# Kernel optimization log

Hardware: AMD Instinct MI355X
Metric: run time of the kernel (lower is better)

Reference implementation:

```python
import jax, jax.numpy as jnp
import numpy as np

D_MODEL = 2048
NUM_HEADS = 32
NUM_GROUPS = 8
D_K = D_MODEL // NUM_HEADS          # 64
HPG = NUM_HEADS // NUM_GROUPS       # heads per group = 4
B, S = 2, 2048


def setup_inputs() -> dict:
    key = jax.random.key(0)
    ks = jax.random.split(key, 9)
    w_scale = 0.02
    kv_dim = NUM_GROUPS * D_K
    return {
        "x":  jax.random.normal(ks[0], (B, S, D_MODEL), dtype=jnp.float32),
        "Wq": jax.random.normal(ks[1], (D_MODEL, D_MODEL), dtype=jnp.float32) * w_scale,
        "bq": jnp.zeros((D_MODEL,), dtype=jnp.float32),
        "Wk": jax.random.normal(ks[2], (D_MODEL, kv_dim), dtype=jnp.float32) * w_scale,
        "bk": jnp.zeros((kv_dim,), dtype=jnp.float32),
        "Wv": jax.random.normal(ks[3], (D_MODEL, kv_dim), dtype=jnp.float32) * w_scale,
        "bv": jnp.zeros((kv_dim,), dtype=jnp.float32),
        "Wo": jax.random.normal(ks[4], (D_MODEL, D_MODEL), dtype=jnp.float32) * w_scale,
        "bo": jnp.zeros((D_MODEL,), dtype=jnp.float32),
    }


def reference(x, Wq, bq, Wk, bk, Wv, bv, Wo, bo):
    b, s, _ = x.shape
    # projections (torch Linear math: x @ W^T + b, here weights stored as (in,out))
    Q = (x @ Wq + bq).reshape(b, s, NUM_HEADS, D_K).transpose(0, 2, 1, 3)   # [B,H,S,dk]
    Kg = (x @ Wk + bk).reshape(b, s, NUM_GROUPS, D_K).transpose(0, 2, 1, 3)  # [B,G,S,dk]
    Vg = (x @ Wv + bv).reshape(b, s, NUM_GROUPS, D_K).transpose(0, 2, 1, 3)
    # repeat_interleave K/V over head dim to full head count
    K = jnp.repeat(Kg, HPG, axis=1)  # [B,H,S,dk]
    V = jnp.repeat(Vg, HPG, axis=1)
    scores = jnp.einsum("bhqd,bhkd->bhqk", Q, K) / np.sqrt(D_K).astype(np.float32)
    attn = jax.nn.softmax(scores, axis=-1)
    out = jnp.einsum("bhqk,bhkd->bhqd", attn, V)               # [B,H,S,dk]
    out = out.transpose(0, 2, 1, 3).reshape(b, s, D_MODEL)
    out = out @ Wo + bo
    # module returns grouped K,V cache: K[:, ::HPG] == Kg
    return out, (Kg, Vg)
```

## Files before the change

kernel.cpp:

```cpp
#include <hip/hip_runtime.h>
#include <hip/hip_bf16.h>
#include <stdint.h>

#define S_LEN 2048
#define DM    2048
#define NH    32
#define NG    8
#define DK    64
#define BATCH 2
#define MROWS (BATCH*S_LEN)
#define NQKV  3072
#define SSCALE 0.18033688f

typedef __bf16 bf16x8 __attribute__((ext_vector_type(8)));
typedef short  s16x8  __attribute__((ext_vector_type(8)));
typedef float  f32x4  __attribute__((ext_vector_type(4)));
typedef unsigned int u32x4 __attribute__((ext_vector_type(4)));

__device__ __forceinline__ unsigned short f2b(float f) {
    unsigned int x = __float_as_uint(f);
    unsigned int r = (x + 0x7fffu + ((x >> 16) & 1u)) >> 16;
    return (unsigned short)r;
}
__device__ __forceinline__ bf16x8 ld8(const unsigned short* p) {
    return *(const bf16x8*)p;
}
__device__ __forceinline__ s16x8 cvt8(const float* p) {
    f32x4 a = *(const f32x4*)p;
    f32x4 b = *(const f32x4*)(p + 4);
    s16x8 o;
#pragma unroll
    for (int j = 0; j < 4; j++) { o[j] = (short)f2b(a[j]); o[4 + j] = (short)f2b(b[j]); }
    return o;
}
__device__ __forceinline__ void gl_lds(const unsigned short* g, unsigned short* l) {
    __builtin_amdgcn_global_load_lds(
        (const __attribute__((address_space(1))) unsigned int*)g,
        (__attribute__((address_space(3))) unsigned int*)l, 16, 0, 0);
}
__device__ __forceinline__ void wait_vm4() {
    asm volatile("s_waitcnt vmcnt(4)" ::: "memory");
}
__device__ __forceinline__ void wait_vm0() {
    asm volatile("s_waitcnt vmcnt(0)" ::: "memory");
}
__device__ __forceinline__ void bar() {
    __builtin_amdgcn_sched_barrier(0);
    __builtin_amdgcn_s_barrier();
    __builtin_amdgcn_sched_barrier(0);
}

#define TCVT 4096
#define TQ   4096
#define TK   1024
#define TV   1024
#define TO   4096
#define TB   12
#define NPREP (TCVT+TQ+TK+TV+TO+TB)
__global__ __launch_bounds__(256) void prep_fused(
    const float* __restrict__ x,
    const float* __restrict__ Wq, const float* __restrict__ Wk,
    const float* __restrict__ Wv, const float* __restrict__ Wo,
    const float* __restrict__ bq, const float* __restrict__ bk,
    const float* __restrict__ bv,
    unsigned short* __restrict__ xb,
    unsigned short* __restrict__ WqkvT, unsigned short* __restrict__ WoT,
    float* __restrict__ bqkv) {
    __shared__ float t[32][33];
    int bid = blockIdx.x;
    const int tx = threadIdx.x, ty = threadIdx.y;
    const int flat = ty * 32 + tx;
    if (bid < TCVT) {
        size_t id = (size_t)bid * 256 + flat;
        *(s16x8*)&xb[id * 8] = cvt8(x + id * 8);
        return;
    }
    bid -= TCVT;
    const float* in; unsigned short* out; int C, bx, by;
    if (bid < TQ) { in = Wq; out = WqkvT; C = DM; bx = bid & 63; by = bid >> 6; }
    else if ((bid -= TQ) < TK) { in = Wk; out = WqkvT + (size_t)2048 * DM; C = 512; bx = bid & 15; by = bid >> 4; }
    else if ((bid -= TK) < TV) { in = Wv; out = WqkvT + (size_t)2560 * DM; C = 512; bx = bid & 15; by = bid >> 4; }
    else if ((bid -= TV) < TO) { in = Wo; out = WoT; C = DM; bx = bid & 63; by = bid >> 6; }
    else {
        int i = (bid - TO) * 256 + flat;
        if (i < 2048) bqkv[i] = bq[i];
        else if (i < 2560) bqkv[i] = bk[i - 2048];
        else if (i < 3072) bqkv[i] = bv[i - 2560];
        return;
    }
    const int R = DM;
    int c0 = bx * 32, r0 = by * 32;
#pragma unroll
    for (int i = 0; i < 4; i++)
        t[ty + i * 8][tx] = in[(size_t)(r0 + ty + i * 8) * C + c0 + tx];
    __syncthreads();
#pragma unroll
    for (int i = 0; i < 4; i++)
        out[(size_t)(c0 + ty + i * 8) * R + r0 + tx] = f2b(t[tx][ty + i * 8]);
}

__device__ __forceinline__ void xcd_remap(int gx, int* bx, int* by) {
    int nwg = gx * (int)gridDim.y;
    int flat = (int)blockIdx.y * gx + (int)blockIdx.x;
    int wgid = (flat & 7) * (nwg >> 3) + (flat >> 3);
    *bx = wgid % gx;
    *by = wgid / gx;
}

__global__ __launch_bounds__(256, 3) void gemm_qkv(const unsigned short* __restrict__ A,
                                                const unsigned short* __restrict__ Bt,
                                                const float* __restrict__ bias,
                                                unsigned short* __restrict__ Qb,
                                                float* __restrict__ Kg, float* __restrict__ Vg,
                                                unsigned short* __restrict__ Kb,
                                                unsigned short* __restrict__ Vtb) {
    __shared__ alignas(16) unsigned short As[3][128 * 32];
    __shared__ alignas(16) unsigned short Bs[3][128 * 32];
    const int K = DM;
    const int tid = threadIdx.x;
    int bx, by;
    xcd_remap(NQKV / 128, &bx, &by);
    const int n0 = bx * 128, m0 = by * 128;
    const int w = tid >> 6, lane = tid & 63;
    const int ln15 = lane & 15, quad = lane >> 4;
    const int wm = (w >> 1) * 64, wn = (w & 1) * 64;
    const int xq = (quad ^ ((ln15 >> 1) & 3)) * 8;
    f32x4 acc[4][4] = {};

#define GSTAGE(k0v, buf) do {                                                    \
    _Pragma("unroll")                                                            \
    for (int i = 0; i < 2; ++i) {                                                \
        int s = w * 128 + i * 64 + lane;             \
        int r = s >> 2, cb = (s & 3) ^ ((r >> 1) & 3);                           \
        gl_lds(&A[(size_t)(m0 + r) * K + (k0v) + cb * 8],                        \
               &As[buf][(w * 128 + i * 64) * 8]);                                \
        gl_lds(&Bt[(size_t)(n0 + r) * K + (k0v) + cb * 8],                       \
               &Bs[buf][(w * 128 + i * 64) * 8]);                                \
    } } while (0)

    GSTAGE(0, 0);
    GSTAGE(32, 1);
    int cur = 0;
    for (int k0 = 0; k0 < K; k0 += 32) {
        if (k0 + 32 < K) wait_vm4(); else wait_vm0();
        bar();
        if (k0 + 64 < K) {
            int nb = cur + 2; if (nb >= 3) nb -= 3;
            GSTAGE(k0 + 64, nb);
        }
        bf16x8 af[4], bfr[4];
#pragma unroll
        for (int mt = 0; mt < 4; mt++)
            af[mt] = ld8(&As[cur][(wm + mt * 16 + ln15) * 32 + xq]);
#pragma unroll
        for (int nt = 0; nt < 4; nt++)
            bfr[nt] = ld8(&Bs[cur][(wn + nt * 16 + ln15) * 32 + xq]);
        __builtin_amdgcn_s_setprio(1);
#pragma unroll
        for (int mt = 0; mt < 4; mt++)
#pragma unroll
            for (int nt = 0; nt < 4; nt++)
                acc[mt][nt] = __builtin_amdgcn_mfma_f32_16x16x32_bf16(af[mt], bfr[nt], acc[mt][nt], 0, 0, 0);
        __builtin_amdgcn_s_setprio(0);
        cur = (cur + 1 == 3) ? 0 : cur + 1;
    }
#undef GSTAGE
#pragma unroll
    for (int nt = 0; nt < 4; nt++) {
        int col = n0 + wn + nt * 16 + ln15;
        float bv = bias[col];
#pragma unroll
        for (int mt = 0; mt < 4; mt++) {
            int row0 = m0 + wm + mt * 16 + quad * 4;
#pragma unroll
            for (int r = 0; r < 4; r++) {
                float val = acc[mt][nt][r] + bv;
                int row = row0 + r;
                int b = row >> 11, s = row & 2047;
                if (col < 2048) {
                    Qb[(size_t)row * DM + col] = f2b(val * SSCALE);
                } else if (col < 2560) {
                    int gc = col - 2048, g = gc >> 6, d = gc & 63;
                    size_t idx = (((size_t)(b * NG + g) * S_LEN + s) << 6) + d;
                    Kg[idx] = val;
                    Kb[idx] = f2b(val);
                } else {
                    int gc = col - 2560, g = gc >> 6, d = gc & 63;
                    Vg[(((size_t)(b * NG + g) * S_LEN + s) << 6) + d] = val;
                    Vtb[((size_t)(b * NG + g) * DK + d) * S_LEN + s] = f2b(val);
                }
            }
        }
    }
}

__global__ __launch_bounds__(256, 3) void gemm_o(const unsigned short* __restrict__ A,
                                              const unsigned short* __restrict__ Bt,
                                              const float* __restrict__ bias,
                                              float* __restrict__ C) {
    __shared__ alignas(16) unsigned short As[3][128 * 32];
    __shared__ alignas(16) unsigned short Bs[3][128 * 32];
    const int K = DM, N = DM;
    const int tid = threadIdx.x;
    int bx, by;
    xcd_remap(DM / 128, &bx, &by);
    const int n0 = bx * 128, m0 = by * 128;
    const int w = tid >> 6, lane = tid & 63;
    const int ln15 = lane & 15, quad = lane >> 4;
    const int wm = (w >> 1) * 64, wn = (w & 1) * 64;
    const int xq = (quad ^ ((ln15 >> 1) & 3)) * 8;
    f32x4 acc[4][4] = {};

#define GSTAGE(k0v, buf) do {                                                    \
    _Pragma("unroll")                                                            \
    for (int i = 0; i < 2; ++i) {                                                \
        int s = w * 128 + i * 64 + lane;                                         \
        int r = s >> 2, cb = (s & 3) ^ ((r >> 1) & 3);                           \
        gl_lds(&A[(size_t)(m0 + r) * K + (k0v) + cb * 8],                        \
               &As[buf][(w * 128 + i * 64) * 8]);                                \
        gl_lds(&Bt[(size_t)(n0 + r) * K + (k0v) + cb * 8],                       \
               &Bs[buf][(w * 128 + i * 64) * 8]);                                \
    } } while (0)

    GSTAGE(0, 0);
    GSTAGE(32, 1);
    int cur = 0;
    for (int k0 = 0; k0 < K; k0 += 32) {
        if (k0 + 32 < K) wait_vm4(); else wait_vm0();
        bar();
        if (k0 + 64 < K) {
            int nb = cur + 2; if (nb >= 3) nb -= 3;
            GSTAGE(k0 + 64, nb);
        }
        bf16x8 af[4], bfr[4];
#pragma unroll
        for (int mt = 0; mt < 4; mt++)
            af[mt] = ld8(&As[cur][(wm + mt * 16 + ln15) * 32 + xq]);
#pragma unroll
        for (int nt = 0; nt < 4; nt++)
            bfr[nt] = ld8(&Bs[cur][(wn + nt * 16 + ln15) * 32 + xq]);
        __builtin_amdgcn_s_setprio(1);
#pragma unroll
        for (int mt = 0; mt < 4; mt++)
#pragma unroll
            for (int nt = 0; nt < 4; nt++)
                acc[mt][nt] = __builtin_amdgcn_mfma_f32_16x16x32_bf16(af[mt], bfr[nt], acc[mt][nt], 0, 0, 0);
        __builtin_amdgcn_s_setprio(0);
        cur = (cur + 1 == 3) ? 0 : cur + 1;
    }
#undef GSTAGE
#pragma unroll
    for (int nt = 0; nt < 4; nt++) {
        int col = n0 + wn + nt * 16 + ln15;
        float bv = bias[col];
#pragma unroll
        for (int mt = 0; mt < 4; mt++) {
            int row0 = m0 + wm + mt * 16 + quad * 4;
#pragma unroll
            for (int r = 0; r < 4; r++)
                C[(size_t)(row0 + r) * N + col] = acc[mt][nt][r] + bv;
        }
    }
}

#define MT 2
__global__ __launch_bounds__(256, 4) void attn_fwd(const unsigned short* __restrict__ Qb,
                                                   const unsigned short* __restrict__ Kb,
                                                   const unsigned short* __restrict__ Vtb,
                                                   unsigned short* __restrict__ AO) {
    __shared__ alignas(16) unsigned short Ks[2][64 * 64];
    __shared__ alignas(16) unsigned short Vt[2][64 * 64];
    const int b = blockIdx.z, h = blockIdx.y, q0 = blockIdx.x * (MT * 64);
    const int g = h >> 2;
    const int tid = threadIdx.x;
    const int w = tid >> 6, lane = tid & 63;
    const int ln15 = lane & 15, quad = lane >> 4;
    const int x7a = (quad ^ (ln15 & 7)) * 8;
    const int x7b = x7a ^ 32;

    bf16x8 aq[MT][2];
#pragma unroll
    for (int mt = 0; mt < MT; mt++) {
        const size_t qrow =
            ((size_t)(b * S_LEN + q0 + w * (MT * 16) + mt * 16 + ln15)) * DM + h * DK;
        aq[mt][0] = ld8(&Qb[qrow + quad * 8]);
        aq[mt][1] = ld8(&Qb[qrow + 32 + quad * 8]);
    }

    bf16x8 ones;
#pragma unroll
    for (int j = 0; j < 8; j++) ones[j] = (__bf16)1.0f;

    f32x4 o[MT][4] = {};
    f32x4 l_acc[MT] = {};
    const size_t kvb = ((size_t)(b * NG + g)) * S_LEN * DK;

#define STAGE(k0v, buf) do {                                                     \
    _Pragma("unroll")                                                            \
    for (int i = 0; i < 2; i++) {                                                \
        int s = w * 128 + i * 64 + lane;                                         \
        int r = s >> 3, cb = (s & 7) ^ (r & 7);                                  \
        gl_lds(&Kb[kvb + (size_t)((k0v) + r) * DK + cb * 8],                     \
               &Ks[buf][(w * 128 + i * 64) * 8]);                                \
        gl_lds(&Vtb[kvb + (size_t)r * S_LEN + (k0v) + cb * 8],                   \
               &Vt[buf][(w * 128 + i * 64) * 8]);                                \
    } } while (0)

    STAGE(0, 0);
    wait_vm0();
    __syncthreads();
    int cur = 0;

    for (int k0 = 0; k0 < S_LEN; k0 += 64) {
        if (k0 + 64 < S_LEN) STAGE(k0 + 64, cur ^ 1);

        f32x4 z[MT][4];
        __builtin_amdgcn_s_setprio(1);
#pragma unroll
        for (int nt = 0; nt < 4; nt++) {
            bf16x8 bk0 = ld8(&Ks[cur][(nt * 16 + ln15) * 64 + x7a]);
            bf16x8 bk1 = ld8(&Ks[cur][(nt * 16 + ln15) * 64 + x7b]);
#pragma unroll
            for (int mt = 0; mt < MT; mt++) {
                f32x4 t = {0.f, 0.f, 0.f, 0.f};
                t = __builtin_amdgcn_mfma_f32_16x16x32_bf16(bk0, aq[mt][0], t, 0, 0, 0);
                t = __builtin_amdgcn_mfma_f32_16x16x32_bf16(bk1, aq[mt][1], t, 0, 0, 0);
                z[mt][nt] = t;
            }
        }
        __builtin_amdgcn_s_setprio(0);

        bf16x8 pa[MT][2];
#pragma unroll
        for (int mt = 0; mt < MT; mt++) {
            unsigned int S[4][2];
#pragma unroll
            for (int nt = 0; nt < 4; nt++) {
                f32x4 pe;
#pragma unroll
                for (int r = 0; r < 4; r++)
                    pe[r] = __builtin_amdgcn_exp2f(z[mt][nt][r]);
                asm("v_cvt_pk_bf16_f32 %0, %1, %2" : "=v"(S[nt][0]) : "v"(pe[0]), "v"(pe[1]));
                asm("v_cvt_pk_bf16_f32 %0, %1, %2" : "=v"(S[nt][1]) : "v"(pe[2]), "v"(pe[3]));
            }
#pragma unroll
            for (int f = 0; f < 2; f++) {
                unsigned int wA[2], wB[2];
#pragma unroll
                for (int p = 0; p < 2; p++) {
                    unsigned int xa = S[2 * f][p], yb = S[2 * f + 1][p];
                    asm("v_permlane32_swap_b32 %0, %1" : "+v"(xa), "+v"(yb));
                    asm("v_permlane16_swap_b32 %0, %1" : "+v"(xa), "+v"(yb));
                    wA[p] = xa; wB[p] = yb;
                }
                u32x4 t4;
                t4[0] = wA[0]; t4[1] = wA[1]; t4[2] = wB[0]; t4[3] = wB[1];
                pa[mt][f] = __builtin_bit_cast(bf16x8, t4);
            }
        }

        __builtin_amdgcn_s_setprio(1);
#pragma unroll
        for (int nt = 0; nt < 4; nt++) {
            bf16x8 bv0 = ld8(&Vt[cur][(nt * 16 + ln15) * 64 + x7a]);
            bf16x8 bv1 = ld8(&Vt[cur][(nt * 16 + ln15) * 64 + x7b]);
#pragma unroll
            for (int mt = 0; mt < MT; mt++) {
                f32x4 t = o[mt][nt];
                t = __builtin_amdgcn_mfma_f32_16x16x32_bf16(pa[mt][0], bv0, t, 0, 0, 0);
                t = __builtin_amdgcn_mfma_f32_16x16x32_bf16(pa[mt][1], bv1, t, 0, 0, 0);
                o[mt][nt] = t;
            }
        }
#pragma unroll
        for (int mt = 0; mt < MT; mt++) {
            l_acc[mt] = __builtin_amdgcn_mfma_f32_16x16x32_bf16(pa[mt][0], ones, l_acc[mt], 0, 0, 0);
            l_acc[mt] = __builtin_amdgcn_mfma_f32_16x16x32_bf16(pa[mt][1], ones, l_acc[mt], 0, 0, 0);
        }
        __builtin_amdgcn_s_setprio(0);

        wait_vm0();
        __syncthreads();
        cur ^= 1;
    }
#undef STAGE

#pragma unroll
    for (int mt = 0; mt < MT; mt++) {
#pragma unroll
        for (int r = 0; r < 4; r++) {
            float inv = 1.0f / l_acc[mt][r];
            int q = q0 + w * (MT * 16) + mt * 16 + quad * 4 + r;
#pragma unroll
            for (int nt = 0; nt < 4; nt++) {
                int col = h * DK + nt * 16 + ln15;
                *(__bf16*)&AO[((size_t)(b * S_LEN + q)) * DM + col] =
                    (__bf16)(o[mt][nt][r] * inv);
            }
        }
    }
}

extern "C" void kernel_launch(void* const* d_in, const int* in_sizes, int n_in,
                              void* d_out, int out_size, void* d_ws, size_t ws_size,
                              hipStream_t stream) {
    const float* x  = (const float*)d_in[0];
    const float* Wq = (const float*)d_in[1];
    const float* bq = (const float*)d_in[2];
    const float* Wk = (const float*)d_in[3];
    const float* bk = (const float*)d_in[4];
    const float* Wv = (const float*)d_in[5];
    const float* bv = (const float*)d_in[6];
    const float* Wo = (const float*)d_in[7];
    const float* bo = (const float*)d_in[8];

    float* out = (float*)d_out;
    float* Kg  = out + (size_t)MROWS * DM;
    float* Vg  = Kg + (size_t)BATCH * NG * S_LEN * DK;

    unsigned short* Qb = (unsigned short*)d_out;

    unsigned short* ws    = (unsigned short*)d_ws;
    unsigned short* WqkvT = ws;
    unsigned short* WoT   = WqkvT + (size_t)NQKV * DM;
    unsigned short* Kb    = WoT + (size_t)DM * DM;
    unsigned short* Vtb   = Kb + (size_t)BATCH * NG * S_LEN * DK;
    unsigned short* AO    = Vtb + (size_t)BATCH * NG * S_LEN * DK;
    unsigned short* xb    = AO + (size_t)MROWS * DM;
    float*          bqkv  = (float*)(xb + (size_t)MROWS * DM);

    hipLaunchKernelGGL(prep_fused, dim3(NPREP), dim3(32, 8), 0, stream,
                       x, Wq, Wk, Wv, Wo, bq, bk, bv, xb, WqkvT, WoT, bqkv);

    hipLaunchKernelGGL(gemm_qkv, dim3(NQKV / 128, MROWS / 128), dim3(256), 0, stream,
                       xb, WqkvT, bqkv, Qb, Kg, Vg, Kb, Vtb);

    hipLaunchKernelGGL(attn_fwd, dim3(S_LEN / (MT * 64), NH, BATCH), dim3(256), 0, stream,
                       Qb, Kb, Vtb, AO);

    hipLaunchKernelGGL(gemm_o, dim3(DM / 128, MROWS / 128), dim3(256), 0, stream,
                       AO, WoT, bo, out);
}
```

Measured before the change: 321.9 us.

## Double M tile and waves per block in GEMMs and attention

```diff
diff --git a/kernel.cpp b/kernel.cpp
--- a/kernel.cpp
+++ b/kernel.cpp
@@ -38,8 +38,8 @@
         (const __attribute__((address_space(1))) unsigned int*)g,
         (__attribute__((address_space(3))) unsigned int*)l, 16, 0, 0);
 }
-__device__ __forceinline__ void wait_vm4() {
-    asm volatile("s_waitcnt vmcnt(4)" ::: "memory");
+__device__ __forceinline__ void wait_vm3() {
+    asm volatile("s_waitcnt vmcnt(3)" ::: "memory");
 }
 __device__ __forceinline__ void wait_vm0() {
     asm volatile("s_waitcnt vmcnt(0)" ::: "memory");
@@ -107,20 +107,20 @@
     *by = wgid / gx;
 }
 
-__global__ __launch_bounds__(256, 3) void gemm_qkv(const unsigned short* __restrict__ A,
+__global__ __launch_bounds__(512, 4) void gemm_qkv(const unsigned short* __restrict__ A,
                                                 const unsigned short* __restrict__ Bt,
                                                 const float* __restrict__ bias,
                                                 unsigned short* __restrict__ Qb,
                                                 float* __restrict__ Kg, float* __restrict__ Vg,
                                                 unsigned short* __restrict__ Kb,
                                                 unsigned short* __restrict__ Vtb) {
-    __shared__ alignas(16) unsigned short As[3][128 * 32];
+    __shared__ alignas(16) unsigned short As[3][256 * 32];
     __shared__ alignas(16) unsigned short Bs[3][128 * 32];
     const int K = DM;
     const int tid = threadIdx.x;
     int bx, by;
     xcd_remap(NQKV / 128, &bx, &by);
-    const int n0 = bx * 128, m0 = by * 128;
+    const int n0 = bx * 128, m0 = by * 256;
     const int w = tid >> 6, lane = tid & 63;
     const int ln15 = lane & 15, quad = lane >> 4;
     const int wm = (w >> 1) * 64, wn = (w & 1) * 64;
@@ -130,19 +130,23 @@
 #define GSTAGE(k0v, buf) do {                                                    \
     _Pragma("unroll")                                                            \
     for (int i = 0; i < 2; ++i) {                                                \
-        int s = w * 128 + i * 64 + lane;             \
+        int s = i * 512 + tid;                   \
         int r = s >> 2, cb = (s & 3) ^ ((r >> 1) & 3);                           \
         gl_lds(&A[(size_t)(m0 + r) * K + (k0v) + cb * 8],                        \
-               &As[buf][(w * 128 + i * 64) * 8]);                                \
+               &As[buf][(i * 512 + w * 64) * 8]);                                \
+    }                                                                            \
+    {                                                                            \
+        int s = tid;                                         \
+        int r = s >> 2, cb = (s & 3) ^ ((r >> 1) & 3);                           \
         gl_lds(&Bt[(size_t)(n0 + r) * K + (k0v) + cb * 8],                       \
-               &Bs[buf][(w * 128 + i * 64) * 8]);                                \
+               &Bs[buf][(w * 64) * 8]);                                          \
     } } while (0)
 
     GSTAGE(0, 0);
     GSTAGE(32, 1);
     int cur = 0;
     for (int k0 = 0; k0 < K; k0 += 32) {
-        if (k0 + 32 < K) wait_vm4(); else wait_vm0();
+        if (k0 + 32 < K) wait_vm3(); else wait_vm0();
         bar();
         if (k0 + 64 < K) {
             int nb = cur + 2; if (nb >= 3) nb -= 3;
@@ -194,17 +198,17 @@
     }
 }
 
-__global__ __launch_bounds__(256, 3) void gemm_o(const unsigned short* __restrict__ A,
+__global__ __launch_bounds__(512, 4) void gemm_o(const unsigned short* __restrict__ A,
                                               const unsigned short* __restrict__ Bt,
                                               const float* __restrict__ bias,
                                               float* __restrict__ C) {
-    __shared__ alignas(16) unsigned short As[3][128 * 32];
+    __shared__ alignas(16) unsigned short As[3][256 * 32];
     __shared__ alignas(16) unsigned short Bs[3][128 * 32];
     const int K = DM, N = DM;
     const int tid = threadIdx.x;
     int bx, by;
     xcd_remap(DM / 128, &bx, &by);
-    const int n0 = bx * 128, m0 = by * 128;
+    const int n0 = bx * 128, m0 = by * 256;
     const int w = tid >> 6, lane = tid & 63;
     const int ln15 = lane & 15, quad = lane >> 4;
     const int wm = (w >> 1) * 64, wn = (w & 1) * 64;
@@ -214,19 +218,23 @@
 #define GSTAGE(k0v, buf) do {                                                    \
     _Pragma("unroll")                                                            \
     for (int i = 0; i < 2; ++i) {                                                \
-        int s = w * 128 + i * 64 + lane;                                         \
+        int s = i * 512 + tid;                                                   \
         int r = s >> 2, cb = (s & 3) ^ ((r >> 1) & 3);                           \
         gl_lds(&A[(size_t)(m0 + r) * K + (k0v) + cb * 8],                        \
-               &As[buf][(w * 128 + i * 64) * 8]);                                \
+               &As[buf][(i * 512 + w * 64) * 8]);                                \
+    }                                                                            \
+    {                                                                            \
+        int s = tid;                                                             \
+        int r = s >> 2, cb = (s & 3) ^ ((r >> 1) & 3);                           \
         gl_lds(&Bt[(size_t)(n0 + r) * K + (k0v) + cb * 8],                       \
-               &Bs[buf][(w * 128 + i * 64) * 8]);                                \
+               &Bs[buf][(w * 64) * 8]);                                          \
     } } while (0)
 
     GSTAGE(0, 0);
     GSTAGE(32, 1);
     int cur = 0;
     for (int k0 = 0; k0 < K; k0 += 32) {
-        if (k0 + 32 < K) wait_vm4(); else wait_vm0();
+        if (k0 + 32 < K) wait_vm3(); else wait_vm0();
         bar();
         if (k0 + 64 < K) {
             int nb = cur + 2; if (nb >= 3) nb -= 3;
@@ -264,13 +272,13 @@
 }
 
 #define MT 2
-__global__ __launch_bounds__(256, 4) void attn_fwd(const unsigned short* __restrict__ Qb,
+__global__ __launch_bounds__(512, 4) void attn_fwd(const unsigned short* __restrict__ Qb,
                                                    const unsigned short* __restrict__ Kb,
                                                    const unsigned short* __restrict__ Vtb,
                                                    unsigned short* __restrict__ AO) {
     __shared__ alignas(16) unsigned short Ks[2][64 * 64];
     __shared__ alignas(16) unsigned short Vt[2][64 * 64];
-    const int b = blockIdx.z, h = blockIdx.y, q0 = blockIdx.x * (MT * 64);
+    const int b = blockIdx.z, h = blockIdx.y, q0 = blockIdx.x * 256;
     const int g = h >> 2;
     const int tid = threadIdx.x;
     const int w = tid >> 6, lane = tid & 63;
@@ -282,7 +290,7 @@
 #pragma unroll
     for (int mt = 0; mt < MT; mt++) {
         const size_t qrow =
-            ((size_t)(b * S_LEN + q0 + w * (MT * 16) + mt * 16 + ln15)) * DM + h * DK;
+            ((size_t)(b * S_LEN + q0 + w * 32 + mt * 16 + ln15)) * DM + h * DK;
         aq[mt][0] = ld8(&Qb[qrow + quad * 8]);
         aq[mt][1] = ld8(&Qb[qrow + 32 + quad * 8]);
     }
@@ -296,15 +304,12 @@
     const size_t kvb = ((size_t)(b * NG + g)) * S_LEN * DK;
 
 #define STAGE(k0v, buf) do {                                                     \
-    _Pragma("unroll")                                                            \
-    for (int i = 0; i < 2; i++) {                                                \
-        int s = w * 128 + i * 64 + lane;                                         \
-        int r = s >> 3, cb = (s & 7) ^ (r & 7);                                  \
-        gl_lds(&Kb[kvb + (size_t)((k0v) + r) * DK + cb * 8],                     \
-               &Ks[buf][(w * 128 + i * 64) * 8]);                                \
-        gl_lds(&Vtb[kvb + (size_t)r * S_LEN + (k0v) + cb * 8],                   \
-               &Vt[buf][(w * 128 + i * 64) * 8]);                                \
-    } } while (0)
+    int r = tid >> 3, cb = (tid & 7) ^ (r & 7);                                  \
+    gl_lds(&Kb[kvb + (size_t)((k0v) + r) * DK + cb * 8],                         \
+           &Ks[buf][(w * 64) * 8]);                                              \
+    gl_lds(&Vtb[kvb + (size_t)r * S_LEN + (k0v) + cb * 8],                       \
+           &Vt[buf][(w * 64) * 8]);                                              \
+    } while (0)
 
     STAGE(0, 0);
     wait_vm0();
@@ -390,7 +395,7 @@
 #pragma unroll
         for (int r = 0; r < 4; r++) {
             float inv = 1.0f / l_acc[mt][r];
-            int q = q0 + w * (MT * 16) + mt * 16 + quad * 4 + r;
+            int q = q0 + w * 32 + mt * 16 + quad * 4 + r;
 #pragma unroll
             for (int nt = 0; nt < 4; nt++) {
                 int col = h * DK + nt * 16 + ln15;
@@ -432,12 +437,12 @@
     hipLaunchKernelGGL(prep_fused, dim3(NPREP), dim3(32, 8), 0, stream,
                        x, Wq, Wk, Wv, Wo, bq, bk, bv, xb, WqkvT, WoT, bqkv);
 
-    hipLaunchKernelGGL(gemm_qkv, dim3(NQKV / 128, MROWS / 128), dim3(256), 0, stream,
+    hipLaunchKernelGGL(gemm_qkv, dim3(NQKV / 128, MROWS / 256), dim3(512), 0, stream,
                        xb, WqkvT, bqkv, Qb, Kg, Vg, Kb, Vtb);
 
-    hipLaunchKernelGGL(attn_fwd, dim3(S_LEN / (MT * 64), NH, BATCH), dim3(256), 0, stream,
+    hipLaunchKernelGGL(attn_fwd, dim3(S_LEN / 256, NH, BATCH), dim3(512), 0, stream,
                        Qb, Kb, Vtb, AO);
 
-    hipLaunchKernelGGL(gemm_o, dim3(DM / 128, MROWS / 128), dim3(256), 0, stream,
+    hipLaunchKernelGGL(gemm_o, dim3(DM / 128, MROWS / 256), dim3(512), 0, stream,
                        AO, WoT, bo, out);
 }
```

After: 326.7 us. About the same (+1.5%).
